# Performance work log

Measured on AMD Instinct MI355X. Metric: run time of the kernel, lower is better.

The kernel has to match this reference:

```python
import jax, jax.numpy as jnp
import numpy as np

B, S, D = 4, 2048, 1024
H = 16
HD = D // H


def setup_inputs() -> dict:
    key = jax.random.key(0)
    ks = jax.random.split(key, 6)
    s = 1.0 / np.sqrt(D)
    x = jax.random.normal(ks[0], (B, S, D), dtype=jnp.float32)
    Wq = jax.random.uniform(ks[1], (D, D), jnp.float32, -s, s)
    Wk = jax.random.uniform(ks[2], (D, D), jnp.float32, -s, s)
    Wv = jax.random.uniform(ks[3], (D, D), jnp.float32, -s, s)
    Wo = jax.random.uniform(ks[4], (D, D), jnp.float32, -s, s)
    bo = jax.random.uniform(ks[5], (D,), jnp.float32, -s, s)
    return {"x": x, "Wq": Wq, "Wk": Wk, "Wv": Wv, "Wo": Wo, "bo": bo}


def reference(x, Wq, Wk, Wv, Wo, bo):
    b, n, _ = x.shape
    # QKV projections (nn.Linear applies x @ W.T; W here stored as [d_in, d_out])
    q = (x @ Wq).reshape(b, n, H, HD).transpose(0, 2, 1, 3)  # [b,h,s,hd]
    k = (x @ Wk).reshape(b, n, H, HD).transpose(0, 2, 1, 3)
    v = (x @ Wv).reshape(b, n, H, HD).transpose(0, 2, 1, 3)
    scores = jnp.einsum('bhqd,bhkd->bhqk', q, k) / np.sqrt(HD).astype(np.float32)
    causal = jnp.tril(jnp.ones((n, n), dtype=bool))  # True = keep
    scores = jnp.where(causal, scores, -jnp.inf)
    attn = jax.nn.softmax(scores, axis=-1)
    ctx = jnp.einsum('bhqk,bhkd->bhqd', attn, v)  # [b,h,s,hd]
    ctx = ctx.transpose(0, 2, 1, 3).reshape(b, n, D)
    return ctx @ Wo + bo
```

## Files before the change

### kernel.cpp

```cpp
#include <hip/hip_runtime.h>

#define NB 4
#define NS 2048
#define ND 1024
#define NH 16
#define NHD 64
#define NTOK (NB*NS)

typedef float f32x4 __attribute__((ext_vector_type(4)));
typedef __bf16 bf16x8 __attribute__((ext_vector_type(8)));
typedef __bf16 bf16x4 __attribute__((ext_vector_type(4)));

#define MFMA16(a,b,c) __builtin_amdgcn_mfma_f32_16x16x32_bf16((a),(b),(c),0,0,0)
#define SBAR() __builtin_amdgcn_s_barrier()
#define VMCNT(n) asm volatile("s_waitcnt vmcnt(" #n ")" ::: "memory")
#define LGKM(n) asm volatile("s_waitcnt lgkmcnt(" #n ")" ::: "memory")
#define SCHEDB() __builtin_amdgcn_sched_barrier(0)

__device__ __forceinline__ void gload_lds16(const __bf16* g, const __bf16* l) {
  __builtin_amdgcn_global_load_lds(
      (const __attribute__((address_space(1))) void*)(uintptr_t)(const void*)g,
      (__attribute__((address_space(3))) void*)(uint32_t)(uintptr_t)(const void*)l,
      16, 0, 0);
}

__global__ void k_convert_x(const float* __restrict__ x, __bf16* __restrict__ xb) {
  int i = blockIdx.x * blockDim.x + threadIdx.x;
  float4 v = ((const float4*)x)[i];
  bf16x4 o = { (__bf16)v.x, (__bf16)v.y, (__bf16)v.z, (__bf16)v.w };
  ((bf16x4*)xb)[i] = o;
}

__global__ void k_transpose_w(const float* __restrict__ w0, const float* __restrict__ w1,
                              const float* __restrict__ w2, const float* __restrict__ w3,
                              __bf16* __restrict__ wqkvt, __bf16* __restrict__ wot) {
  __shared__ float tl[64][65];
  const int z = blockIdx.z;
  const float* src = (z==0)?w0:(z==1)?w1:(z==2)?w2:w3;
  __bf16* dst = (z<3) ? (wqkvt + (size_t)z*ND*ND) : wot;
  const int kb = blockIdx.x*64, nb = blockIdx.y*64;
  const int c = threadIdx.x & 63, r0 = threadIdx.x >> 6;
  for (int i=0;i<16;i++) { int r = r0*16+i; tl[r][c] = src[(size_t)(kb+r)*ND + nb + c]; }
  __syncthreads();
  for (int i=0;i<16;i++) { int r = r0*16+i; dst[(size_t)(nb+r)*ND + kb + c] = (__bf16)tl[c][r]; }
}

__global__ __launch_bounds__(512, 2) void k_gemm_qkv(
    const __bf16* __restrict__ A, const __bf16* __restrict__ Bt,
    __bf16* __restrict__ qs, __bf16* __restrict__ ks, __bf16* __restrict__ vt) {
  constexpr int BUFE = (256+128)*64;
  __shared__ __align__(16) __bf16 lds[3*BUFE];
  const int tid = threadIdx.x;
  const int wid = tid>>6, lane = tid&63;
  const int wr = wid>>1, wc = wid&1;
  const int lrow = lane&15, lg = lane>>4;
  const int srow = lane>>3;
  const int scol = ((lane&7) ^ srow)*8;

  const int id  = blockIdx.x;
  const int xcd = id & 7;
  const int nl  = id >> 3;
  const int st  = nl >> 5;
  const int u   = nl & 31;
  const int bx  = xcd*4 + (u >> 3);
  const int by  = st*8 + (u & 7);
  const int m0 = bx*256, n0 = by*128;

  auto stage = [&](int t, int bsel) {
    __bf16* buf = lds + bsel*BUFE;
    const int k0 = t*64;
    #pragma unroll
    for (int i=0;i<4;i++) {
      int c = wid + i*8;
      gload_lds16(A + (size_t)(m0 + c*8 + srow)*ND + k0 + scol, buf + c*512);
    }
    #pragma unroll
    for (int i=0;i<2;i++) {
      int c = wid + i*8;
      gload_lds16(Bt + (size_t)(n0 + c*8 + srow)*ND + k0 + scol, buf + 16384 + c*512);
    }
  };

  int kx[8];
  #pragma unroll
  for (int kk=0;kk<8;kk++) kx[kk] = ((kk ^ (lrow&7)) << 4);
  const int abase = (wr*64 + lrow)*128;
  const int bbase = 32768 + (wc*64 + lrow)*128;

  f32x4 acc[4][4];
  f32x4 zero = {0.f,0.f,0.f,0.f};
  #pragma unroll
  for (int i=0;i<4;i++) for (int j=0;j<4;j++) acc[i][j] = zero;

  stage(0,0);
  stage(1,1);
  for (int t=0; t<16; ++t) {
    if (t < 14) stage(t+2, (t+2)%3);
    if (t < 14)      { VMCNT(12); }
    else if (t == 14){ VMCNT(6);  }
    else             { VMCNT(0);  }
    SBAR();
    const char* L = (const char*)(lds + (t%3)*BUFE);
    bf16x8 bfr[4][2], af[4][2];
    #pragma unroll
    for (int cb=0;cb<4;cb++)
      #pragma unroll
      for (int ksi=0;ksi<2;ksi++)
        bfr[cb][ksi] = *(const bf16x8*)(L + bbase + cb*2048 + kx[ksi*4+lg]);
    #pragma unroll
    for (int mf=0;mf<2;mf++)
      #pragma unroll
      for (int ksi=0;ksi<2;ksi++)
        af[mf][ksi] = *(const bf16x8*)(L + abase + mf*2048 + kx[ksi*4+lg]);
    SCHEDB();
    #pragma unroll
    for (int mf=2;mf<4;mf++)
      #pragma unroll
      for (int ksi=0;ksi<2;ksi++)
        af[mf][ksi] = *(const bf16x8*)(L + abase + mf*2048 + kx[ksi*4+lg]);
    LGKM(4);
    SCHEDB();
    __builtin_amdgcn_s_setprio(1);
    #pragma unroll
    for (int mf=0;mf<2;mf++)
      #pragma unroll
      for (int cb=0;cb<4;cb++)
        #pragma unroll
        for (int ksi=0;ksi<2;ksi++)
          acc[mf][cb] = MFMA16(af[mf][ksi], bfr[cb][ksi], acc[mf][cb]);
    __builtin_amdgcn_s_setprio(0);
    LGKM(0);
    SCHEDB();
    __builtin_amdgcn_s_setprio(1);
    #pragma unroll
    for (int mf=2;mf<4;mf++)
      #pragma unroll
      for (int cb=0;cb<4;cb++)
        #pragma unroll
        for (int ksi=0;ksi<2;ksi++)
          acc[mf][cb] = MFMA16(af[mf][ksi], bfr[cb][ksi], acc[mf][cb]);
    __builtin_amdgcn_s_setprio(0);
    SBAR();
  }

  const int which = by >> 3;
  const int h = (by&7)*2 + wc;
  __bf16* ws = lds + wid*4096;
  const int tokbase = m0 + wr*64;
  const int b = tokbase >> 11, s0 = tokbase & 2047;

  if (which < 2) {
    __bf16* dst = which ? ks : qs;
    #pragma unroll
    for (int mf=0;mf<4;mf++)
      #pragma unroll
      for (int cb=0;cb<4;cb++)
        #pragma unroll
        for (int r=0;r<4;r++) {
          int row = mf*16 + lg*4 + r;
          int chunk = (cb*2 + (lrow>>3)) ^ (row&7);
          *(__bf16*)((char*)ws + row*128 + chunk*16 + (lrow&7)*2) = (__bf16)acc[mf][cb][r];
        }
    #pragma unroll
    for (int p=0;p<8;p++) {
      int row = p*8 + (lane>>3);
      int chunk = (lane&7) ^ (row&7);
      bf16x8 v = *(const bf16x8*)((char*)ws + row*128 + chunk*16);
      *(bf16x8*)(dst + ((size_t)(b*NH + h)*NS + s0 + row)*NHD + (lane&7)*8) = v;
    }
  } else {
    #pragma unroll
    for (int mf=0;mf<4;mf++)
      #pragma unroll
      for (int cb=0;cb<4;cb++) {
        bf16x4 pk = { (__bf16)acc[mf][cb][0], (__bf16)acc[mf][cb][1],
                      (__bf16)acc[mf][cb][2], (__bf16)acc[mf][cb][3] };
        int ldsrow = cb*16 + lrow;
        int chunk = (mf*2 + (lg>>1)) ^ (ldsrow&7);
        *(bf16x4*)((char*)ws + ldsrow*128 + chunk*16 + (lg&1)*8) = pk;
      }
    #pragma unroll
    for (int p=0;p<8;p++) {
      int hd = p*8 + (lane>>3);
      int chunk = (lane&7) ^ (hd&7);
      bf16x8 v = *(const bf16x8*)((char*)ws + hd*128 + chunk*16);
      *(bf16x8*)(vt + ((size_t)(b*NH + h)*NHD + hd)*NS + s0 + (lane&7)*8) = v;
    }
  }
}

template<int BM>
__device__ __forceinline__ void gemm_mainloop(
    const __bf16* __restrict__ Ag, const __bf16* __restrict__ Bg,
    int m0, int n0, __bf16* lds, f32x4 (&acc)[BM/32][4])
{
  constexpr int MF   = BM/32;
  constexpr int MFH  = MF/2;
  constexpr int LA   = BM/64;
  constexpr int LB   = 4;
  constexpr int BUFE = (BM+256)*64;
  const int tid = threadIdx.x;
  const int wid = tid>>6, lane = tid&63;
  const int wr = wid>>2, wc = wid&3;
  const int lrow = lane&15, lg = lane>>4;
  const int srow = lane>>3;
  const int scol = ((lane&7) ^ srow) * 8;

  auto stage = [&](int t, int buf) {
    const int k0 = t*64;
    __bf16* dstA = lds + buf*BUFE;
    __bf16* dstB = dstA + BM*64;
    #pragma unroll
    for (int i=0;i<LA;i++) {
      int c = wid + i*8;
      gload_lds16(Ag + (size_t)(m0 + c*8 + srow)*ND + k0 + scol, dstA + c*512);
    }
    #pragma unroll
    for (int i=0;i<LB;i++) {
      int c = wid + i*8;
      gload_lds16(Bg + (size_t)(n0 + c*8 + srow)*ND + k0 + scol, dstB + c*512);
    }
  };

  int kx[8];
  #pragma unroll
  for (int kk=0;kk<8;kk++) kx[kk] = ((kk ^ (lrow&7)) << 4);
  const int abase = (wr*(BM/2) + lrow)*128;
  const int bbase = BM*128 + (wc*64 + lrow)*128;

  bf16x8 af[MFH][2];
  bf16x8 bfr[4][2];

  auto phase = [&](const char* L, int q) {
    const int mq = q>>1, nq = q&1;
    if (q == 0 || q == 2) {
      #pragma unroll
      for (int m=0;m<MFH;m++)
        #pragma unroll
        for (int ksi=0;ksi<2;ksi++)
          af[m][ksi] = *(const bf16x8*)(L + abase + (mq*MFH+m)*2048 + kx[ksi*4+lg]);
    }
    if (q == 0 || q == 1) {
      #pragma unroll
      for (int n=0;n<2;n++)
        #pragma unroll
        for (int ksi=0;ksi<2;ksi++)
          bfr[q*2+n][ksi] = *(const bf16x8*)(L + bbase + (q*2+n)*2048 + kx[ksi*4+lg]);
    }
    SBAR();
    LGKM(0);
    SCHEDB();
    __builtin_amdgcn_s_setprio(1);
    #pragma unroll
    for (int m=0;m<MFH;m++)
      #pragma unroll
      for (int n=0;n<2;n++)
        #pragma unroll
        for (int ksi=0;ksi<2;ksi++)
          acc[mq*MFH+m][nq*2+n] = MFMA16(af[m][ksi], bfr[nq*2+n][ksi], acc[mq*MFH+m][nq*2+n]);
    __builtin_amdgcn_s_setprio(0);
    SBAR();
  };

  stage(0, 0);
  for (int j=0;j<8;j++) {
    stage(2*j+1, 1);
    if constexpr (LA+LB == 8) { VMCNT(8); } else { VMCNT(6); }
    SBAR();
    #pragma unroll
    for (int q=0;q<4;q++) phase((const char*)lds, q);
    if (j < 7) {
      stage(2*j+2, 0);
      if constexpr (LA+LB == 8) { VMCNT(8); } else { VMCNT(6); }
    } else {
      VMCNT(0);
    }
    SBAR();
    #pragma unroll
    for (int q=0;q<4;q++) phase((const char*)(lds + BUFE), q);
  }
}

__global__ __launch_bounds__(512, 2) void k_gemm_out(
    const __bf16* __restrict__ A, const __bf16* __restrict__ Bt,
    const float* __restrict__ bo, float* __restrict__ out) {
  __shared__ __align__(16) __bf16 lds[2*(128+256)*64];
  const int id = blockIdx.x;
  const int nid = (id&7)*32 + (id>>3);
  const int bx = nid>>2, by = nid&3;
  const int m0 = bx*128, n0 = by*256;

  f32x4 acc[4][4];
  f32x4 zero = {0.f,0.f,0.f,0.f};
  #pragma unroll
  for (int i=0;i<4;i++) for (int j=0;j<4;j++) acc[i][j] = zero;

  gemm_mainloop<128>(A, Bt, m0, n0, lds, acc);

  const int wid = threadIdx.x>>6, lane = threadIdx.x&63;
  const int wr = wid>>2, wc = wid&3, lrow = lane&15, lg = lane>>4;
  #pragma unroll
  for (int cb=0;cb<4;cb++) {
    const int n = n0 + wc*64 + cb*16 + lrow;
    const float bias = bo[n];
    #pragma unroll
    for (int mf=0;mf<4;mf++)
      #pragma unroll
      for (int r=0;r<4;r++) {
        const int m = m0 + wr*64 + mf*16 + lg*4 + r;
        out[(size_t)m*ND + n] = acc[mf][cb][r] + bias;
      }
  }
}

__global__ __launch_bounds__(256, 3) void k_attn(
    const __bf16* __restrict__ qs, const __bf16* __restrict__ ks,
    const __bf16* __restrict__ vt, __bf16* __restrict__ ctx) {
  __shared__ __align__(16) __bf16 sK[2][64*64];
  __shared__ __align__(16) __bf16 sV[2][64*64];
  __shared__ __align__(16) __bf16 sP[4][32*72];
  const int tid = threadIdx.x, w = tid >> 6, lane = tid & 63;
  const int lrow = lane & 15, lg = lane >> 4;
  const int bh = blockIdx.x;
  const int bq = 15 - blockIdx.y;
  const int nt = 2*bq + 2;
  const size_t base = (size_t)bh * NS * NHD;
  const __bf16* Kg = ks + base;
  const __bf16* Vg = vt + base;
  __bf16* sPw = sP[w];

  const int q0w = bq*128 + w*32;
  bf16x8 qf[2][2];
  for (int rb=0;rb<2;rb++)
    for (int kk=0;kk<2;kk++) {
      bf16x8 v = *(const bf16x8*)(qs + base + (size_t)(q0w + rb*16 + lrow)*NHD + kk*32 + lg*8);
      bf16x8 o;
      for (int j=0;j<8;j++) o[j] = (__bf16)((float)v[j] * 0.125f);
      qf[rb][kk] = o;
    }

  int koffB[4][2];
  for (int cb=0;cb<4;cb++) {
    int r = cb*16 + lrow;
    for (int kk=0;kk<2;kk++)
      koffB[cb][kk] = r*128 + (((kk*4 + lg) ^ (r & 7)) << 4);
  }
  const int s_r[2]  = { (w + 0)*8 + (lane>>3), (w + 4)*8 + (lane>>3) };
  const int s_u[2]  = { (lane&7) ^ (s_r[0]&7), (lane&7) ^ (s_r[1]&7) };

  f32x4 zero = {0.f,0.f,0.f,0.f};
  f32x4 oacc[2][4];
  float psum[2][4];
  for (int rb=0;rb<2;rb++){ for(int cb=0;cb<4;cb++) oacc[rb][cb]=zero;
                            for(int r=0;r<4;r++) psum[rb][r]=0.f; }

  for (int i=0;i<2;i++) {
    gload_lds16(Kg + (size_t)s_r[i]*NHD + s_u[i]*8,              sK[0] + (w + i*4)*512);
    gload_lds16(Vg + (size_t)s_r[i]*NS  + s_u[i]*8,              sV[0] + (w + i*4)*512);
  }
  asm volatile("s_waitcnt vmcnt(0)" ::: "memory");
  __syncthreads();

  int buf = 0;
  for (int t = 0; t < nt; ++t) {
    if (t+1 < nt) {
      const __bf16* Kt = Kg + (size_t)(t+1)*64*NHD;
      for (int i=0;i<2;i++) {
        gload_lds16(Kt + (size_t)s_r[i]*NHD + s_u[i]*8,          sK[buf^1] + (w + i*4)*512);
        gload_lds16(Vg + (size_t)s_r[i]*NS + (t+1)*64 + s_u[i]*8, sV[buf^1] + (w + i*4)*512);
      }
    }
    if (!(t == nt-1 && w < 2)) {
      const __bf16* bK = sK[buf];
      const __bf16* bV = sV[buf];
      const bool bdry = (t >= nt-2);
      for (int cb=0;cb<4;cb++) {
        bf16x8 kf0 = *(const bf16x8*)((const char*)bK + koffB[cb][0]);
        bf16x8 kf1 = *(const bf16x8*)((const char*)bK + koffB[cb][1]);
        const int kv = t*64 + cb*16 + lrow;
        for (int rb=0;rb<2;rb++) {
          f32x4 s4 = MFMA16(qf[rb][0], kf0, zero);
          s4 = MFMA16(qf[rb][1], kf1, s4);
          const int qrow = q0w + rb*16 + lg*4;
          for (int r=0;r<4;r++) {
            float e = __expf(s4[r]);
            if (bdry && kv > qrow + r) e = 0.f;
            psum[rb][r] += e;
            sPw[(rb*16 + lg*4 + r)*72 + cb*16 + lrow] = (__bf16)e;
          }
        }
      }
      for (int kk=0;kk<2;kk++) {
        bf16x8 pa0 = *(const bf16x8*)(sPw + (lrow)*72      + kk*32 + lg*8);
        bf16x8 pa1 = *(const bf16x8*)(sPw + (16 + lrow)*72 + kk*32 + lg*8);
        for (int cb=0;cb<4;cb++) {
          bf16x8 vb = *(const bf16x8*)((const char*)bV + koffB[cb][kk]);
          oacc[0][cb] = MFMA16(pa0, vb, oacc[0][cb]);
          oacc[1][cb] = MFMA16(pa1, vb, oacc[1][cb]);
        }
      }
    }
    asm volatile("s_waitcnt vmcnt(0)" ::: "memory");
    __syncthreads();
    buf ^= 1;
  }

  for (int rb=0;rb<2;rb++) for (int r=0;r<4;r++) {
    float s = psum[rb][r];
    for (int off=1; off<16; off<<=1) s += __shfl_xor(s, off);
    psum[rb][r] = 1.0f / s;
  }

  __bf16* ws = &sK[0][0] + w*2048;
  for (int rb=0;rb<2;rb++)
    for (int cb=0;cb<4;cb++)
      for (int r=0;r<4;r++) {
        int row = rb*16 + lg*4 + r;
        int chunk = (cb*2 + (lrow>>3)) ^ (row&7);
        *(__bf16*)((char*)ws + row*128 + chunk*16 + (lrow&7)*2) =
            (__bf16)(oacc[rb][cb][r] * psum[rb][r]);
      }
  const int b = bh >> 4, h = bh & 15;
  for (int p=0;p<4;p++) {
    int row = p*8 + (lane>>3);
    int chunk = (lane&7) ^ (row&7);
    bf16x8 v = *(const bf16x8*)((char*)ws + row*128 + chunk*16);
    int q = q0w + row;
    *(bf16x8*)(ctx + ((size_t)(b*NS + q))*ND + h*NHD + (lane&7)*8) = v;
  }
}

extern "C" void kernel_launch(void* const* d_in, const int* in_sizes, int n_in,
                              void* d_out, int out_size, void* d_ws, size_t ws_size,
                              hipStream_t stream) {
  const float* x  = (const float*)d_in[0];
  const float* Wq = (const float*)d_in[1];
  const float* Wk = (const float*)d_in[2];
  const float* Wv = (const float*)d_in[3];
  const float* Wo = (const float*)d_in[4];
  const float* bo = (const float*)d_in[5];
  float* out = (float*)d_out;

  __bf16* xb    = (__bf16*)d_ws;
  __bf16* wqkvt = xb    + (size_t)NTOK*ND;
  __bf16* wot   = wqkvt + (size_t)3*ND*ND;
  __bf16* qsc   = wot   + (size_t)ND*ND;
  __bf16* ksc   = qsc   + (size_t)NTOK*ND;
  __bf16* vtc   = ksc   + (size_t)NTOK*ND;
  __bf16* ctx   = vtc   + (size_t)NTOK*ND;

  k_convert_x<<<NTOK*ND/(4*256), 256, 0, stream>>>(x, xb);
  k_transpose_w<<<dim3(ND/64, ND/64, 4), 256, 0, stream>>>(Wq, Wk, Wv, Wo, wqkvt, wot);
  k_gemm_qkv<<<768, 512, 0, stream>>>(xb, wqkvt, qsc, ksc, vtc);
  k_attn<<<dim3(NB*NH, NS/128), 256, 0, stream>>>(qsc, ksc, vtc, ctx);
  k_gemm_out<<<256, 512, 0, stream>>>(ctx, wot, bo, out);
}
```

Baseline: 158.7 us.

## Rewrite output GEMM with triple-buffered 256x128 tiles and use exp2 in attention

The output-projection GEMM drops the shared templated mainloop and gets its own loop. It uses 256x128 block tiles on a 4x2 wave grid with a three-stage LDS ring buffer, split LDS-read waits that overlap fragment loads with MFMAs, and a new XCD-aware block mapping. In attention, the Q pre-scale now folds in log2(e) so the softmax can call the hardware exp2 instruction directly instead of __expf. The deeper buffering raises LDS use per block, which may limit occupancy under the 2-block launch bound.

```diff
diff --git a/kernel.cpp b/kernel.cpp
--- a/kernel.cpp
+++ b/kernel.cpp
@@ -16,6 +16,14 @@
 #define VMCNT(n) asm volatile("s_waitcnt vmcnt(" #n ")" ::: "memory")
 #define LGKM(n) asm volatile("s_waitcnt lgkmcnt(" #n ")" ::: "memory")
 #define SCHEDB() __builtin_amdgcn_sched_barrier(0)
+
+__device__ __forceinline__ float fexp2(float x) {
+#if __has_builtin(__builtin_amdgcn_exp2f)
+  return __builtin_amdgcn_exp2f(x);
+#else
+  return __expf(x * 0.69314718056f);
+#endif
+}
 
 __device__ __forceinline__ void gload_lds16(const __bf16* g, const __bf16* l) {
   __builtin_amdgcn_global_load_lds(
@@ -189,116 +197,102 @@
   }
 }
 
-template<int BM>
-__device__ __forceinline__ void gemm_mainloop(
-    const __bf16* __restrict__ Ag, const __bf16* __restrict__ Bg,
-    int m0, int n0, __bf16* lds, f32x4 (&acc)[BM/32][4])
-{
-  constexpr int MF   = BM/32;
-  constexpr int MFH  = MF/2;
-  constexpr int LA   = BM/64;
-  constexpr int LB   = 4;
-  constexpr int BUFE = (BM+256)*64;
+__global__ __launch_bounds__(512, 2) void k_gemm_out(
+    const __bf16* __restrict__ A, const __bf16* __restrict__ Bt,
+    const float* __restrict__ bo, float* __restrict__ out) {
+  constexpr int BUFE = (256+128)*64;
+  __shared__ __align__(16) __bf16 lds[3*BUFE];
   const int tid = threadIdx.x;
   const int wid = tid>>6, lane = tid&63;
-  const int wr = wid>>2, wc = wid&3;
+  const int wr = wid>>1, wc = wid&1;
   const int lrow = lane&15, lg = lane>>4;
   const int srow = lane>>3;
-  const int scol = ((lane&7) ^ srow) * 8;
-
-  auto stage = [&](int t, int buf) {
+  const int scol = ((lane&7) ^ srow)*8;
+
+  const int id  = blockIdx.x;
+  const int xcd = id & 7;
+  const int nl  = id >> 3;
+  const int bx  = xcd*4 + (nl >> 3);
+  const int by  = nl & 7;
+  const int m0 = bx*256, n0 = by*128;
+
+  auto stage = [&](int t, int bsel) {
+    __bf16* buf = lds + bsel*BUFE;
     const int k0 = t*64;
-    __bf16* dstA = lds + buf*BUFE;
-    __bf16* dstB = dstA + BM*64;
-    #pragma unroll
-    for (int i=0;i<LA;i++) {
+    #pragma unroll
+    for (int i=0;i<4;i++) {
       int c = wid + i*8;
-      gload_lds16(Ag + (size_t)(m0 + c*8 + srow)*ND + k0 + scol, dstA + c*512);
-    }
-    #pragma unroll
-    for (int i=0;i<LB;i++) {
+      gload_lds16(A + (size_t)(m0 + c*8 + srow)*ND + k0 + scol, buf + c*512);
+    }
+    #pragma unroll
+    for (int i=0;i<2;i++) {
       int c = wid + i*8;
-      gload_lds16(Bg + (size_t)(n0 + c*8 + srow)*ND + k0 + scol, dstB + c*512);
+      gload_lds16(Bt + (size_t)(n0 + c*8 + srow)*ND + k0 + scol, buf + 16384 + c*512);
     }
   };
 
   int kx[8];
   #pragma unroll
   for (int kk=0;kk<8;kk++) kx[kk] = ((kk ^ (lrow&7)) << 4);
-  const int abase = (wr*(BM/2) + lrow)*128;
-  const int bbase = BM*128 + (wc*64 + lrow)*128;
-
-  bf16x8 af[MFH][2];
-  bf16x8 bfr[4][2];
-
-  auto phase = [&](const char* L, int q) {
-    const int mq = q>>1, nq = q&1;
-    if (q == 0 || q == 2) {
-      #pragma unroll
-      for (int m=0;m<MFH;m++)
-        #pragma unroll
-        for (int ksi=0;ksi<2;ksi++)
-          af[m][ksi] = *(const bf16x8*)(L + abase + (mq*MFH+m)*2048 + kx[ksi*4+lg]);
-    }
-    if (q == 0 || q == 1) {
-      #pragma unroll
-      for (int n=0;n<2;n++)
-        #pragma unroll
-        for (int ksi=0;ksi<2;ksi++)
-          bfr[q*2+n][ksi] = *(const bf16x8*)(L + bbase + (q*2+n)*2048 + kx[ksi*4+lg]);
-    }
-    SBAR();
-    LGKM(0);
-    SCHEDB();
-    __builtin_amdgcn_s_setprio(1);
-    #pragma unroll
-    for (int m=0;m<MFH;m++)
-      #pragma unroll
-      for (int n=0;n<2;n++)
-        #pragma unroll
-        for (int ksi=0;ksi<2;ksi++)
-          acc[mq*MFH+m][nq*2+n] = MFMA16(af[m][ksi], bfr[nq*2+n][ksi], acc[mq*MFH+m][nq*2+n]);
-    __builtin_amdgcn_s_setprio(0);
-    SBAR();
-  };
-
-  stage(0, 0);
-  for (int j=0;j<8;j++) {
-    stage(2*j+1, 1);
-    if constexpr (LA+LB == 8) { VMCNT(8); } else { VMCNT(6); }
-    SBAR();
-    #pragma unroll
-    for (int q=0;q<4;q++) phase((const char*)lds, q);
-    if (j < 7) {
-      stage(2*j+2, 0);
-      if constexpr (LA+LB == 8) { VMCNT(8); } else { VMCNT(6); }
-    } else {
-      VMCNT(0);
-    }
-    SBAR();
-    #pragma unroll
-    for (int q=0;q<4;q++) phase((const char*)(lds + BUFE), q);
-  }
-}
-
-__global__ __launch_bounds__(512, 2) void k_gemm_out(
-    const __bf16* __restrict__ A, const __bf16* __restrict__ Bt,
-    const float* __restrict__ bo, float* __restrict__ out) {
-  __shared__ __align__(16) __bf16 lds[2*(128+256)*64];
-  const int id = blockIdx.x;
-  const int nid = (id&7)*32 + (id>>3);
-  const int bx = nid>>2, by = nid&3;
-  const int m0 = bx*128, n0 = by*256;
+  const int abase = (wr*64 + lrow)*128;
+  const int bbase = 32768 + (wc*64 + lrow)*128;
 
   f32x4 acc[4][4];
   f32x4 zero = {0.f,0.f,0.f,0.f};
   #pragma unroll
   for (int i=0;i<4;i++) for (int j=0;j<4;j++) acc[i][j] = zero;
 
-  gemm_mainloop<128>(A, Bt, m0, n0, lds, acc);
-
-  const int wid = threadIdx.x>>6, lane = threadIdx.x&63;
-  const int wr = wid>>2, wc = wid&3, lrow = lane&15, lg = lane>>4;
+  stage(0,0);
+  stage(1,1);
+  for (int t=0; t<16; ++t) {
+    if (t < 14) stage(t+2, (t+2)%3);
+    if (t < 14)      { VMCNT(12); }
+    else if (t == 14){ VMCNT(6);  }
+    else             { VMCNT(0);  }
+    SBAR();
+    const char* L = (const char*)(lds + (t%3)*BUFE);
+    bf16x8 bfr[4][2], af[4][2];
+    #pragma unroll
+    for (int cb=0;cb<4;cb++)
+      #pragma unroll
+      for (int ksi=0;ksi<2;ksi++)
+        bfr[cb][ksi] = *(const bf16x8*)(L + bbase + cb*2048 + kx[ksi*4+lg]);
+    #pragma unroll
+    for (int mf=0;mf<2;mf++)
+      #pragma unroll
+      for (int ksi=0;ksi<2;ksi++)
+        af[mf][ksi] = *(const bf16x8*)(L + abase + mf*2048 + kx[ksi*4+lg]);
+    SCHEDB();
+    #pragma unroll
+    for (int mf=2;mf<4;mf++)
+      #pragma unroll
+      for (int ksi=0;ksi<2;ksi++)
+        af[mf][ksi] = *(const bf16x8*)(L + abase + mf*2048 + kx[ksi*4+lg]);
+    LGKM(4);
+    SCHEDB();
+    __builtin_amdgcn_s_setprio(1);
+    #pragma unroll
+    for (int mf=0;mf<2;mf++)
+      #pragma unroll
+      for (int cb=0;cb<4;cb++)
+        #pragma unroll
+        for (int ksi=0;ksi<2;ksi++)
+          acc[mf][cb] = MFMA16(af[mf][ksi], bfr[cb][ksi], acc[mf][cb]);
+    __builtin_amdgcn_s_setprio(0);
+    LGKM(0);
+    SCHEDB();
+    __builtin_amdgcn_s_setprio(1);
+    #pragma unroll
+    for (int mf=2;mf<4;mf++)
+      #pragma unroll
+      for (int cb=0;cb<4;cb++)
+        #pragma unroll
+        for (int ksi=0;ksi<2;ksi++)
+          acc[mf][cb] = MFMA16(af[mf][ksi], bfr[cb][ksi], acc[mf][cb]);
+    __builtin_amdgcn_s_setprio(0);
+    SBAR();
+  }
+
   #pragma unroll
   for (int cb=0;cb<4;cb++) {
     const int n = n0 + wc*64 + cb*16 + lrow;
@@ -335,7 +329,7 @@
     for (int kk=0;kk<2;kk++) {
       bf16x8 v = *(const bf16x8*)(qs + base + (size_t)(q0w + rb*16 + lrow)*NHD + kk*32 + lg*8);
       bf16x8 o;
-      for (int j=0;j<8;j++) o[j] = (__bf16)((float)v[j] * 0.125f);
+      for (int j=0;j<8;j++) o[j] = (__bf16)((float)v[j] * 0.1803368801f);
       qf[rb][kk] = o;
     }
 
@@ -383,7 +377,7 @@
           s4 = MFMA16(qf[rb][1], kf1, s4);
           const int qrow = q0w + rb*16 + lg*4;
           for (int r=0;r<4;r++) {
-            float e = __expf(s4[r]);
+            float e = fexp2(s4[r]);
             if (bdry && kv > qrow + r) e = 0.f;
             psum[rb][r] += e;
             sPw[(rb*16 + lg*4 + r)*72 + cb*16 + lrow] = (__bf16)e;
```

Result: no change. 157.3 us (-0.9%).
